# Optimization experiments

Measured on AMD Instinct MI355X. Metric: run time of the kernel, lower is better.

The kernel has to match this reference:

```python
import jax, jax.numpy as jnp
import numpy as np

NEG = -1e9

def setup_inputs() -> dict:
    key = jax.random.key(0)
    ks = jax.random.split(key, 6)
    B, T, H = 32, 2048, 1024
    dec = jax.random.normal(ks[0], (B, H), dtype=jnp.float32)
    enc = jax.random.normal(ks[1], (B, T, H), dtype=jnp.float32)
    mask = jax.random.randint(ks[2], (B, T), 0, 2).astype(jnp.int32)
    scale = 1.0 / np.sqrt(H)
    W_enc = jax.random.normal(ks[3], (H, H), dtype=jnp.float32) * scale
    W_dec = jax.random.normal(ks[4], (H, H), dtype=jnp.float32) * scale
    v = jax.random.normal(ks[5], (H,), dtype=jnp.float32) * scale
    return {"decoder_hidden": dec, "encoder_outputs": enc, "mask": mask,
            "W_enc": W_enc, "W_dec": W_dec, "v": v}

def reference(decoder_hidden, encoder_outputs, mask, W_enc, W_dec, v):
    # enc proj: [B,T,H] @ W_enc^T ; dec proj: [B,H] @ W_dec^T broadcast over T
    enc_p = jnp.einsum('bth,oh->bto', encoder_outputs, W_enc)
    dec_p = jnp.einsum('bh,oh->bo', decoder_hidden, W_dec)[:, None, :]  # [B,1,H]
    energy = jnp.tanh(enc_p + dec_p)                                    # [B,T,H]
    scores = jnp.einsum('bth,h->bt', energy, v)                         # [B,T]
    scores = jnp.where(mask == 0, NEG, scores)
    attn_weights = jax.nn.softmax(scores, axis=1)                       # [B,T]
    context = jnp.einsum('bt,bth->bh', attn_weights, encoder_outputs)   # [B,H]
    return (context, attn_weights)
```

## Files before the change

### kernel.cpp

```cpp
#include <hip/hip_runtime.h>
#include <hip/hip_bf16.h>
#include <stdint.h>

#define B_ 32
#define T_ 2048
#define H_ 1024
#define M_ (B_*T_)

typedef __bf16 bf16x8 __attribute__((ext_vector_type(8)));
typedef float  f32x4  __attribute__((ext_vector_type(4)));

__device__ __forceinline__ float tanh_fast(float x) {
    float e = __expf(2.0f * x);
    return 1.0f - 2.0f / (e + 1.0f);
}

__global__ __launch_bounds__(256) void k_decp(const float* __restrict__ dec,
                                              const float* __restrict__ Wd,
                                              float* __restrict__ decp) {
    int bx = blockIdx.x;
    int b = bx & 31, oc = bx >> 5;
    int tid = threadIdx.x;
    int o = oc * 64 + (tid >> 2);
    int kq = tid & 3;
    const f32x4* wr = (const f32x4*)&Wd[(size_t)o * H_ + kq * 256];
    const f32x4* dr = (const f32x4*)&dec[(size_t)b * H_ + kq * 256];
    f32x4 s4 = {0.f, 0.f, 0.f, 0.f};
#pragma unroll 8
    for (int i = 0; i < 64; ++i) s4 += wr[i] * dr[i];
    float s = s4[0] + s4[1] + s4[2] + s4[3];
    s += __shfl_xor(s, 1);
    s += __shfl_xor(s, 2);
    if (kq == 0) decp[b * H_ + o] = s;
}

__global__ __launch_bounds__(256) void k_wtile(const float* __restrict__ We,
                                               __bf16* __restrict__ Wt) {
    int tg = blockIdx.x * 256 + threadIdx.x;
    int kk = tg >> 12;
    int ng = (tg >> 6) & 63;
    int lane = tg & 63;
    int rr = lane & 15, qq = lane >> 4;
    int o = ng * 16 + rr;
    int k = kk * 32 + qq * 8;
    const f32x4* src = (const f32x4*)&We[(size_t)o * H_ + k];
    f32x4 f0 = src[0], f1 = src[1];
    bf16x8 h;
    h[0] = (__bf16)f0[0]; h[1] = (__bf16)f0[1]; h[2] = (__bf16)f0[2]; h[3] = (__bf16)f0[3];
    h[4] = (__bf16)f1[0]; h[5] = (__bf16)f1[1]; h[6] = (__bf16)f1[2]; h[7] = (__bf16)f1[3];
    *(bf16x8*)&Wt[(size_t)tg * 8] = h;
}

__global__ __launch_bounds__(256, 3) void k_scores(const float* __restrict__ enc,
                                                   const float* __restrict__ decp,
                                                   const __bf16* __restrict__ Wt,
                                                   const float* __restrict__ v,
                                                   float* __restrict__ scores) {
    __shared__ __bf16 A_lds[64 * 256];
    __shared__ float red[4][64];

    const int tid = threadIdx.x;
    const int w = tid >> 6, lane = tid & 63;
    const int r = lane & 15, quad = lane >> 4;

    const int bx = blockIdx.x;
    const int xs = bx & 7;
    const int q = bx >> 3;
    const int nt = q & 3;
    const int rg = (q >> 2) * 8 + xs;
    const int m0 = rg * 64;
    const int b = m0 >> 11;
    const int ngbase = nt * 16 + w * 4;

    float dp[4], vvv[4];
#pragma unroll
    for (int j = 0; j < 4; ++j) {
        int col = nt * 256 + w * 64 + j * 16 + r;
        dp[j]  = decp[b * H_ + col];
        vvv[j] = v[col];
    }

    f32x4 acc[4][4];
#pragma unroll
    for (int i = 0; i < 4; ++i)
#pragma unroll
        for (int j = 0; j < 4; ++j) {
            f32x4 z; z[0] = dp[j]; z[1] = dp[j]; z[2] = dp[j]; z[3] = dp[j];
            acc[i][j] = z;
        }

    const int rg8 = tid >> 5;
    const int tt  = tid & 31;
    const int ks_s = tt >> 2;
    const int lq  = tt & 3;

    bf16x8 b_cur[4];
#pragma unroll
    for (int j = 0; j < 4; ++j)
        b_cur[j] = *(const bf16x8*)&Wt[(((size_t)0 * 64 + ngbase + j) * 64 + lane) * 8];

#pragma unroll 1
    for (int kc = 0; kc < 4; ++kc) {
        {
            const float* srow = &enc[(size_t)(m0 + rg8 * 8) * H_ + kc * 256 + tt * 8];
#pragma unroll
            for (int i = 0; i < 8; ++i) {
                const f32x4* s4 = (const f32x4*)(srow + (size_t)i * H_);
                f32x4 f0 = s4[0], f1 = s4[1];
                bf16x8 h;
                h[0] = (__bf16)f0[0]; h[1] = (__bf16)f0[1]; h[2] = (__bf16)f0[2]; h[3] = (__bf16)f0[3];
                h[4] = (__bf16)f1[0]; h[5] = (__bf16)f1[1]; h[6] = (__bf16)f1[2]; h[7] = (__bf16)f1[3];
                int row = rg8 * 8 + i;
                int mg = row >> 4, rr = row & 15;
                int cell = (ks_s * 4 + mg) * 64 + lq * 16 + ((rr + ks_s) & 15);
                *(bf16x8*)&A_lds[cell * 8] = h;
            }
        }
        __syncthreads();

#pragma unroll
        for (int ks = 0; ks < 8; ++ks) {
            int kk = kc * 8 + ks;
            int kkn = (kk + 1) & 31;
            bf16x8 b_nxt[4];
#pragma unroll
            for (int j = 0; j < 4; ++j)
                b_nxt[j] = *(const bf16x8*)&Wt[(((size_t)kkn * 64 + ngbase + j) * 64 + lane) * 8];

            bf16x8 af[4];
            const int L = (lane & 48) | ((lane + ks) & 15);
#pragma unroll
            for (int i = 0; i < 4; ++i)
                af[i] = *(const bf16x8*)&A_lds[((ks * 4 + i) * 64 + L) * 8];

#pragma unroll
            for (int i = 0; i < 4; ++i)
#pragma unroll
                for (int j = 0; j < 4; ++j)
                    acc[i][j] = __builtin_amdgcn_mfma_f32_16x16x32_bf16(af[i], b_cur[j], acc[i][j], 0, 0, 0);

#pragma unroll
            for (int j = 0; j < 4; ++j) b_cur[j] = b_nxt[j];
        }
        __syncthreads();
    }

    float sp[4][4];
#pragma unroll
    for (int i = 0; i < 4; ++i)
#pragma unroll
        for (int g = 0; g < 4; ++g) sp[i][g] = 0.f;

#pragma unroll
    for (int i = 0; i < 4; ++i)
#pragma unroll
        for (int j = 0; j < 4; ++j)
#pragma unroll
            for (int g = 0; g < 4; ++g)
                sp[i][g] += tanh_fast(acc[i][j][g]) * vvv[j];

#pragma unroll
    for (int i = 0; i < 4; ++i)
#pragma unroll
        for (int g = 0; g < 4; ++g) {
            float s = sp[i][g];
            s += __shfl_xor(s, 1);
            s += __shfl_xor(s, 2);
            s += __shfl_xor(s, 4);
            s += __shfl_xor(s, 8);
            sp[i][g] = s;
        }

    if (r == 0) {
#pragma unroll
        for (int i = 0; i < 4; ++i)
#pragma unroll
            for (int g = 0; g < 4; ++g)
                red[w][i * 16 + quad * 4 + g] = sp[i][g];
    }
    __syncthreads();
    if (tid < 64) {
        float s = red[0][tid] + red[1][tid] + red[2][tid] + red[3][tid];
        atomicAdd(&scores[m0 + tid], s);
    }
}

__global__ __launch_bounds__(256) void k_softmax(const float* __restrict__ scores,
                                                 const int* __restrict__ mask,
                                                 float* __restrict__ attn) {
    int b = blockIdx.x;
    int tid = threadIdx.x;
    int w = tid >> 6, lane = tid & 63;
    __shared__ float sm[2][4];
    float val[8];
    float mx = -3e38f;
#pragma unroll
    for (int ii = 0; ii < 8; ++ii) {
        int t = tid + ii * 256;
        float s = scores[b * T_ + t];
        s = (mask[b * T_ + t] == 0) ? -1e9f : s;
        val[ii] = s;
        mx = fmaxf(mx, s);
    }
#pragma unroll
    for (int m = 1; m <= 32; m <<= 1) mx = fmaxf(mx, __shfl_xor(mx, m));
    if (lane == 0) sm[0][w] = mx;
    __syncthreads();
    mx = fmaxf(fmaxf(sm[0][0], sm[0][1]), fmaxf(sm[0][2], sm[0][3]));
    float lsum = 0.f;
#pragma unroll
    for (int ii = 0; ii < 8; ++ii) {
        val[ii] = __expf(val[ii] - mx);
        lsum += val[ii];
    }
#pragma unroll
    for (int m = 1; m <= 32; m <<= 1) lsum += __shfl_xor(lsum, m);
    if (lane == 0) sm[1][w] = lsum;
    __syncthreads();
    float inv = 1.0f / (sm[1][0] + sm[1][1] + sm[1][2] + sm[1][3]);
#pragma unroll
    for (int ii = 0; ii < 8; ++ii)
        attn[b * T_ + tid + ii * 256] = val[ii] * inv;
}

__global__ __launch_bounds__(256) void k_context(const float* __restrict__ enc,
                                                 const float* __restrict__ attn,
                                                 float* __restrict__ ctx) {
    int bx = blockIdx.x;
    int b = bx >> 4;
    int sub = bx & 15;
    int hc = sub & 3;
    int tq = sub >> 2;
    int tid = threadIdx.x;
    int wv = tid >> 6, lane = tid & 63;
    int h4 = hc * 256 + lane * 4;
    int t0 = tq * 512 + wv * 128;
    f32x4 acc = {0.f, 0.f, 0.f, 0.f};
#pragma unroll 4
    for (int i = 0; i < 128; ++i) {
        int t = t0 + i;
        float a = attn[b * T_ + t];
        f32x4 e = *(const f32x4*)&enc[((size_t)(b * T_ + t)) * H_ + h4];
        acc += a * e;
    }
    float* out = &ctx[b * H_ + h4];
    atomicAdd(&out[0], acc[0]);
    atomicAdd(&out[1], acc[1]);
    atomicAdd(&out[2], acc[2]);
    atomicAdd(&out[3], acc[3]);
}

extern "C" void kernel_launch(void* const* d_in, const int* in_sizes, int n_in,
                              void* d_out, int out_size, void* d_ws, size_t ws_size,
                              hipStream_t stream) {
    (void)in_sizes; (void)n_in; (void)out_size; (void)ws_size;
    const float* dec  = (const float*)d_in[0];
    const float* enc  = (const float*)d_in[1];
    const int*   mask = (const int*)d_in[2];
    const float* We   = (const float*)d_in[3];
    const float* Wd   = (const float*)d_in[4];
    const float* v    = (const float*)d_in[5];

    float* out = (float*)d_out;
    char* ws = (char*)d_ws;
    float*  decp   = (float*)ws;
    float*  scores = (float*)(ws + 131072);
    __bf16* Wt     = (__bf16*)(ws + 131072 + 262144);

    hipMemsetAsync(out, 0, (size_t)B_ * H_ * sizeof(float), stream);
    hipMemsetAsync(scores, 0, (size_t)M_ * sizeof(float), stream);

    k_decp   <<<512, 256, 0, stream>>>(dec, Wd, decp);
    k_wtile  <<<512, 256, 0, stream>>>(We, Wt);
    k_scores <<<4096, 256, 0, stream>>>(enc, decp, Wt, v, scores);
    k_softmax<<<32, 256, 0, stream>>>(scores, mask, out + B_ * H_);
    k_context<<<512, 256, 0, stream>>>(enc, out + B_ * H_, out);
}
```

Measured before the change: 595.6 us.

## Switch scores GEMM to 32x32 MFMA, fuse prep kernels, drop context atomics

The scores kernel moves from 16x16x32 to 32x32x16 bf16 MFMA tiles with a new weight tiling and XOR-swizzled LDS layout. The A tile is staged per 256-wide K chunk in 32 KB of LDS, and occupancy is raised to 4 blocks. The two prep kernels (weight bf16 tiling and decoder projection) are merged into one launch. The context kernel reduces across waves in LDS and writes directly, removing the output memset and atomics but using fewer, larger blocks.

```diff
diff --git a/kernel.cpp b/kernel.cpp
--- a/kernel.cpp
+++ b/kernel.cpp
@@ -9,59 +9,61 @@
 
 typedef __bf16 bf16x8 __attribute__((ext_vector_type(8)));
 typedef float  f32x4  __attribute__((ext_vector_type(4)));
+typedef float  f32x16 __attribute__((ext_vector_type(16)));
 
 __device__ __forceinline__ float tanh_fast(float x) {
     float e = __expf(2.0f * x);
     return 1.0f - 2.0f / (e + 1.0f);
 }
 
-__global__ __launch_bounds__(256) void k_decp(const float* __restrict__ dec,
+__global__ __launch_bounds__(256) void k_prep(const float* __restrict__ We,
+                                              __bf16* __restrict__ Wt,
+                                              const float* __restrict__ dec,
                                               const float* __restrict__ Wd,
                                               float* __restrict__ decp) {
     int bx = blockIdx.x;
-    int b = bx & 31, oc = bx >> 5;
     int tid = threadIdx.x;
-    int o = oc * 64 + (tid >> 2);
-    int kq = tid & 3;
-    const f32x4* wr = (const f32x4*)&Wd[(size_t)o * H_ + kq * 256];
-    const f32x4* dr = (const f32x4*)&dec[(size_t)b * H_ + kq * 256];
-    f32x4 s4 = {0.f, 0.f, 0.f, 0.f};
+    if (bx < 512) {
+        int tg = bx * 256 + tid;
+        int lane = tg & 63;
+        int c = (tg >> 6) & 31;
+        int s = tg >> 11;
+        int o = c * 32 + (lane & 31);
+        int k = s * 16 + (lane >> 5) * 8;
+        const f32x4* src = (const f32x4*)&We[(size_t)o * H_ + k];
+        f32x4 f0 = src[0], f1 = src[1];
+        bf16x8 h;
+        h[0] = (__bf16)f0[0]; h[1] = (__bf16)f0[1]; h[2] = (__bf16)f0[2]; h[3] = (__bf16)f0[3];
+        h[4] = (__bf16)f1[0]; h[5] = (__bf16)f1[1]; h[6] = (__bf16)f1[2]; h[7] = (__bf16)f1[3];
+        *(bf16x8*)&Wt[(size_t)tg * 8] = h;
+    } else {
+        int bxd = bx - 512;
+        int b = bxd & 31, oc = bxd >> 5;
+        int o = oc * 64 + (tid >> 2);
+        int kq = tid & 3;
+        const f32x4* wr = (const f32x4*)&Wd[(size_t)o * H_ + kq * 256];
+        const f32x4* dr = (const f32x4*)&dec[(size_t)b * H_ + kq * 256];
+        f32x4 s4 = {0.f, 0.f, 0.f, 0.f};
 #pragma unroll 8
-    for (int i = 0; i < 64; ++i) s4 += wr[i] * dr[i];
-    float s = s4[0] + s4[1] + s4[2] + s4[3];
-    s += __shfl_xor(s, 1);
-    s += __shfl_xor(s, 2);
-    if (kq == 0) decp[b * H_ + o] = s;
-}
-
-__global__ __launch_bounds__(256) void k_wtile(const float* __restrict__ We,
-                                               __bf16* __restrict__ Wt) {
-    int tg = blockIdx.x * 256 + threadIdx.x;
-    int kk = tg >> 12;
-    int ng = (tg >> 6) & 63;
-    int lane = tg & 63;
-    int rr = lane & 15, qq = lane >> 4;
-    int o = ng * 16 + rr;
-    int k = kk * 32 + qq * 8;
-    const f32x4* src = (const f32x4*)&We[(size_t)o * H_ + k];
-    f32x4 f0 = src[0], f1 = src[1];
-    bf16x8 h;
-    h[0] = (__bf16)f0[0]; h[1] = (__bf16)f0[1]; h[2] = (__bf16)f0[2]; h[3] = (__bf16)f0[3];
-    h[4] = (__bf16)f1[0]; h[5] = (__bf16)f1[1]; h[6] = (__bf16)f1[2]; h[7] = (__bf16)f1[3];
-    *(bf16x8*)&Wt[(size_t)tg * 8] = h;
-}
-
-__global__ __launch_bounds__(256, 3) void k_scores(const float* __restrict__ enc,
+        for (int i = 0; i < 64; ++i) s4 += wr[i] * dr[i];
+        float s = s4[0] + s4[1] + s4[2] + s4[3];
+        s += __shfl_xor(s, 1);
+        s += __shfl_xor(s, 2);
+        if (kq == 0) decp[b * H_ + o] = s;
+    }
+}
+
+__global__ __launch_bounds__(256, 4) void k_scores(const float* __restrict__ enc,
                                                    const float* __restrict__ decp,
                                                    const __bf16* __restrict__ Wt,
                                                    const float* __restrict__ v,
                                                    float* __restrict__ scores) {
-    __shared__ __bf16 A_lds[64 * 256];
+    __shared__ __bf16 A_lds[64 * 32 * 8];
     __shared__ float red[4][64];
 
     const int tid = threadIdx.x;
     const int w = tid >> 6, lane = tid & 63;
-    const int r = lane & 15, quad = lane >> 4;
+    const int l5 = lane & 31, q2 = lane >> 5;
 
     const int bx = blockIdx.x;
     const int xs = bx & 7;
@@ -70,113 +72,108 @@
     const int rg = (q >> 2) * 8 + xs;
     const int m0 = rg * 64;
     const int b = m0 >> 11;
-    const int ngbase = nt * 16 + w * 4;
-
-    float dp[4], vvv[4];
-#pragma unroll
-    for (int j = 0; j < 4; ++j) {
-        int col = nt * 256 + w * 64 + j * 16 + r;
-        dp[j]  = decp[b * H_ + col];
-        vvv[j] = v[col];
-    }
-
-    f32x4 acc[4][4];
-#pragma unroll
-    for (int i = 0; i < 4; ++i)
-#pragma unroll
-        for (int j = 0; j < 4; ++j) {
-            f32x4 z; z[0] = dp[j]; z[1] = dp[j]; z[2] = dp[j]; z[3] = dp[j];
-            acc[i][j] = z;
-        }
-
-    const int rg8 = tid >> 5;
-    const int tt  = tid & 31;
-    const int ks_s = tt >> 2;
-    const int lq  = tt & 3;
-
-    bf16x8 b_cur[4];
-#pragma unroll
-    for (int j = 0; j < 4; ++j)
-        b_cur[j] = *(const bf16x8*)&Wt[(((size_t)0 * 64 + ngbase + j) * 64 + lane) * 8];
+    const int cg0 = nt * 8 + w * 2;
+
+    float dp[2], vvv[2];
+#pragma unroll
+    for (int ct = 0; ct < 2; ++ct) {
+        int col = (cg0 + ct) * 32 + l5;
+        dp[ct]  = decp[b * H_ + col];
+        vvv[ct] = v[col];
+    }
+
+    f32x16 acc[2][2];
+#pragma unroll
+    for (int rt = 0; rt < 2; ++rt)
+#pragma unroll
+        for (int ct = 0; ct < 2; ++ct)
+#pragma unroll
+            for (int g = 0; g < 16; ++g)
+                acc[rt][ct][g] = dp[ct];
+
+    const int ko_s = tid & 31;
+    const int rbase = (tid >> 5) * 8;
+
+    bf16x8 b_cur[2];
+#pragma unroll
+    for (int ct = 0; ct < 2; ++ct)
+        b_cur[ct] = *(const bf16x8*)&Wt[(((size_t)0 * 32 + cg0 + ct) * 64 + lane) * 8];
 
 #pragma unroll 1
     for (int kc = 0; kc < 4; ++kc) {
         {
-            const float* srow = &enc[(size_t)(m0 + rg8 * 8) * H_ + kc * 256 + tt * 8];
+            const float* sp0 = &enc[(size_t)(m0 + rbase) * H_ + kc * 256 + ko_s * 8];
 #pragma unroll
             for (int i = 0; i < 8; ++i) {
-                const f32x4* s4 = (const f32x4*)(srow + (size_t)i * H_);
+                const f32x4* s4 = (const f32x4*)(sp0 + (size_t)i * H_);
                 f32x4 f0 = s4[0], f1 = s4[1];
                 bf16x8 h;
                 h[0] = (__bf16)f0[0]; h[1] = (__bf16)f0[1]; h[2] = (__bf16)f0[2]; h[3] = (__bf16)f0[3];
                 h[4] = (__bf16)f1[0]; h[5] = (__bf16)f1[1]; h[6] = (__bf16)f1[2]; h[7] = (__bf16)f1[3];
-                int row = rg8 * 8 + i;
-                int mg = row >> 4, rr = row & 15;
-                int cell = (ks_s * 4 + mg) * 64 + lq * 16 + ((rr + ks_s) & 15);
+                int row = rbase + i;
+                int cell = row * 32 + ((ko_s & 24) | ((ko_s ^ row) & 7));
                 *(bf16x8*)&A_lds[cell * 8] = h;
             }
         }
         __syncthreads();
 
 #pragma unroll
-        for (int ks = 0; ks < 8; ++ks) {
-            int kk = kc * 8 + ks;
-            int kkn = (kk + 1) & 31;
-            bf16x8 b_nxt[4];
-#pragma unroll
-            for (int j = 0; j < 4; ++j)
-                b_nxt[j] = *(const bf16x8*)&Wt[(((size_t)kkn * 64 + ngbase + j) * 64 + lane) * 8];
-
-            bf16x8 af[4];
-            const int L = (lane & 48) | ((lane + ks) & 15);
-#pragma unroll
-            for (int i = 0; i < 4; ++i)
-                af[i] = *(const bf16x8*)&A_lds[((ks * 4 + i) * 64 + L) * 8];
-
-#pragma unroll
-            for (int i = 0; i < 4; ++i)
-#pragma unroll
-                for (int j = 0; j < 4; ++j)
-                    acc[i][j] = __builtin_amdgcn_mfma_f32_16x16x32_bf16(af[i], b_cur[j], acc[i][j], 0, 0, 0);
-
-#pragma unroll
-            for (int j = 0; j < 4; ++j) b_cur[j] = b_nxt[j];
+        for (int sl = 0; sl < 16; ++sl) {
+            int s = kc * 16 + sl;
+            int sn = (s + 1) & 63;
+            bf16x8 b_nxt[2];
+#pragma unroll
+            for (int ct = 0; ct < 2; ++ct)
+                b_nxt[ct] = *(const bf16x8*)&Wt[(((size_t)sn * 32 + cg0 + ct) * 64 + lane) * 8];
+
+            bf16x8 af[2];
+#pragma unroll
+            for (int rt = 0; rt < 2; ++rt) {
+                int row = rt * 32 + l5;
+                int ko = sl * 2 + q2;
+                int cell = row * 32 + ((ko & 24) | ((ko ^ row) & 7));
+                af[rt] = *(const bf16x8*)&A_lds[cell * 8];
+            }
+
+            acc[0][0] = __builtin_amdgcn_mfma_f32_32x32x16_bf16(af[0], b_cur[0], acc[0][0], 0, 0, 0);
+            acc[0][1] = __builtin_amdgcn_mfma_f32_32x32x16_bf16(af[0], b_cur[1], acc[0][1], 0, 0, 0);
+            acc[1][0] = __builtin_amdgcn_mfma_f32_32x32x16_bf16(af[1], b_cur[0], acc[1][0], 0, 0, 0);
+            acc[1][1] = __builtin_amdgcn_mfma_f32_32x32x16_bf16(af[1], b_cur[1], acc[1][1], 0, 0, 0);
+
+            b_cur[0] = b_nxt[0];
+            b_cur[1] = b_nxt[1];
         }
         __syncthreads();
     }
 
-    float sp[4][4];
-#pragma unroll
-    for (int i = 0; i < 4; ++i)
-#pragma unroll
-        for (int g = 0; g < 4; ++g) sp[i][g] = 0.f;
-
-#pragma unroll
-    for (int i = 0; i < 4; ++i)
-#pragma unroll
-        for (int j = 0; j < 4; ++j)
-#pragma unroll
-            for (int g = 0; g < 4; ++g)
-                sp[i][g] += tanh_fast(acc[i][j][g]) * vvv[j];
-
-#pragma unroll
-    for (int i = 0; i < 4; ++i)
-#pragma unroll
-        for (int g = 0; g < 4; ++g) {
-            float s = sp[i][g];
+    float sp[2][16];
+#pragma unroll
+    for (int rt = 0; rt < 2; ++rt)
+#pragma unroll
+        for (int g = 0; g < 16; ++g)
+            sp[rt][g] = tanh_fast(acc[rt][0][g]) * vvv[0] + tanh_fast(acc[rt][1][g]) * vvv[1];
+
+#pragma unroll
+    for (int rt = 0; rt < 2; ++rt)
+#pragma unroll
+        for (int g = 0; g < 16; ++g) {
+            float s = sp[rt][g];
             s += __shfl_xor(s, 1);
             s += __shfl_xor(s, 2);
             s += __shfl_xor(s, 4);
             s += __shfl_xor(s, 8);
-            sp[i][g] = s;
+            s += __shfl_xor(s, 16);
+            sp[rt][g] = s;
         }
 
-    if (r == 0) {
-#pragma unroll
-        for (int i = 0; i < 4; ++i)
-#pragma unroll
-            for (int g = 0; g < 4; ++g)
-                red[w][i * 16 + quad * 4 + g] = sp[i][g];
+    if (l5 == 0) {
+#pragma unroll
+        for (int rt = 0; rt < 2; ++rt)
+#pragma unroll
+            for (int g = 0; g < 16; ++g) {
+                int row = rt * 32 + (g & 3) + 8 * (g >> 2) + 4 * q2;
+                red[w][row] = sp[rt][g];
+            }
     }
     __syncthreads();
     if (tid < 64) {
@@ -223,31 +220,35 @@
         attn[b * T_ + tid + ii * 256] = val[ii] * inv;
 }
 
-__global__ __launch_bounds__(256) void k_context(const float* __restrict__ enc,
+__global__ __launch_bounds__(512) void k_context(const float* __restrict__ enc,
                                                  const float* __restrict__ attn,
                                                  float* __restrict__ ctx) {
+    __shared__ f32x4 cred[8][32];
     int bx = blockIdx.x;
-    int b = bx >> 4;
-    int sub = bx & 15;
-    int hc = sub & 3;
-    int tq = sub >> 2;
+    int b = bx >> 3, hc = bx & 7;
     int tid = threadIdx.x;
     int wv = tid >> 6, lane = tid & 63;
-    int h4 = hc * 256 + lane * 4;
-    int t0 = tq * 512 + wv * 128;
+    int l5 = lane & 31, tq2 = lane >> 5;
+    int h = hc * 128 + l5 * 4;
+    const float* ap = &attn[b * T_ + wv * 256 + tq2];
+    const float* ep = &enc[((size_t)b * T_ + wv * 256 + tq2) * H_ + h];
     f32x4 acc = {0.f, 0.f, 0.f, 0.f};
-#pragma unroll 4
+#pragma unroll 8
     for (int i = 0; i < 128; ++i) {
-        int t = t0 + i;
-        float a = attn[b * T_ + t];
-        f32x4 e = *(const f32x4*)&enc[((size_t)(b * T_ + t)) * H_ + h4];
+        float a = ap[2 * i];
+        f32x4 e = *(const f32x4*)(ep + (size_t)2 * i * H_);
         acc += a * e;
     }
-    float* out = &ctx[b * H_ + h4];
-    atomicAdd(&out[0], acc[0]);
-    atomicAdd(&out[1], acc[1]);
-    atomicAdd(&out[2], acc[2]);
-    atomicAdd(&out[3], acc[3]);
+#pragma unroll
+    for (int c = 0; c < 4; ++c) acc[c] += __shfl_xor(acc[c], 32);
+    if (tq2 == 0) cred[wv][l5] = acc;
+    __syncthreads();
+    if (tid < 32) {
+        f32x4 r = cred[0][tid];
+#pragma unroll
+        for (int j = 1; j < 8; ++j) r += cred[j][tid];
+        *(f32x4*)&ctx[b * H_ + hc * 128 + tid * 4] = r;
+    }
 }
 
 extern "C" void kernel_launch(void* const* d_in, const int* in_sizes, int n_in,
@@ -267,12 +268,10 @@
     float*  scores = (float*)(ws + 131072);
     __bf16* Wt     = (__bf16*)(ws + 131072 + 262144);
 
-    hipMemsetAsync(out, 0, (size_t)B_ * H_ * sizeof(float), stream);
     hipMemsetAsync(scores, 0, (size_t)M_ * sizeof(float), stream);
 
-    k_decp   <<<512, 256, 0, stream>>>(dec, Wd, decp);
-    k_wtile  <<<512, 256, 0, stream>>>(We, Wt);
+    k_prep   <<<1024, 256, 0, stream>>>(We, Wt, dec, Wd, decp);
     k_scores <<<4096, 256, 0, stream>>>(enc, decp, Wt, v, scores);
     k_softmax<<<32, 256, 0, stream>>>(scores, mask, out + B_ * H_);
-    k_context<<<512, 256, 0, stream>>>(enc, out + B_ * H_, out);
-}
+    k_context<<<256, 512, 0, stream>>>(enc, out + B_ * H_, out);
+}
```

Result: no change. 588.5 us (-1.2%).
